# Performance work log

Hardware: AMD Instinct MI355X
Metric: run time of the kernel (lower is better)

## Reference

```python
import jax, jax.numpy as jnp
import numpy as np

N = 50000        # nodes
E = 800000       # edges (avg degree 16)
HID = 256        # hidden_size
HEADS = 8        # num_heads
HD = HID // HEADS  # head_dim = 32


def setup_inputs() -> dict:
    key = jax.random.key(0)
    ks = jax.random.split(key, 10)
    h = jax.random.normal(ks[0], (N, HID), dtype=jnp.float32)
    val = jax.random.uniform(ks[1], (E,), dtype=jnp.float32)
    Wq = jax.random.normal(ks[2], (HID, HID), dtype=jnp.float32) * 0.02
    Wk = jax.random.normal(ks[3], (HID, HID), dtype=jnp.float32) * 0.02
    Wv = jax.random.normal(ks[4], (HID, HID), dtype=jnp.float32) * 0.02
    bq = jnp.zeros((HID,), dtype=jnp.float32)
    bk = jnp.zeros((HID,), dtype=jnp.float32)
    bv = jnp.zeros((HID,), dtype=jnp.float32)
    # CSR rows expanded to per-edge row ids (sorted, like row_ptr expansion)
    edge_rows = jnp.sort(jax.random.randint(ks[5], (E,), 0, N, dtype=jnp.int32))
    col_ind = jax.random.randint(ks[6], (E,), 0, N, dtype=jnp.int32)
    return {"h": h, "val": val, "Wq": Wq, "bq": bq, "Wk": Wk, "bk": bk,
            "Wv": Wv, "bv": bv, "edge_rows": edge_rows, "col_ind": col_ind}


def reference(h, val, Wq, bq, Wk, bk, Wv, bv, edge_rows, col_ind):
    scaling = HD ** (-0.5)
    # projections; reshape splits hidden as (head_dim, heads) with heads fastest,
    # exactly as in the torch module: reshape(N, head_dim, num_heads)
    q = ((h @ Wq + bq).reshape(N, HD, HEADS)) * scaling
    k = (h @ Wk + bk).reshape(N, HD, HEADS)
    v = (h @ Wv + bv).reshape(N, HD, HEADS)

    # SDDMM restricted to edges: score[e, head] = <q[row_e], k[col_e]> * A.val[e]
    score = jnp.einsum('edh,edh->eh', q[edge_rows], k[col_ind]) * val[:, None]  # [E, HEADS]

    # per-destination-row softmax over incident edges (stable, segment ops)
    m = jax.ops.segment_max(score, edge_rows, num_segments=N)        # [N, HEADS]
    m = jnp.where(jnp.isfinite(m), m, jnp.zeros_like(m))             # empty rows
    e = jnp.exp(score - m[edge_rows])                                # [E, HEADS]
    denom = jax.ops.segment_sum(e, edge_rows, num_segments=N)        # [N, HEADS]
    attn = e / denom[edge_rows]

    # SpMM: out[i] = sum over edges (i, j) of attn * v[j]
    contrib = attn[:, None, :] * v[col_ind]                          # [E, HD, HEADS]
    out = jax.ops.segment_sum(contrib, edge_rows, num_segments=N)    # [N, HD, HEADS]
    return out.reshape(N, -1)                                        # [N, HID]
```

## Files before the change

### kernel.cpp

```cpp
#include <hip/hip_runtime.h>
#include <hip/hip_bf16.h>
#include <math.h>

static constexpr int kN   = 50000;
static constexpr int kE   = 800000;
static constexpr int kHID = 256;
static constexpr int kHD  = 32;

typedef short bf16x8 __attribute__((ext_vector_type(8)));
typedef float f32x4  __attribute__((ext_vector_type(4)));
typedef unsigned short us8 __attribute__((ext_vector_type(8)));

__device__ __forceinline__ float b2f(unsigned short u) {
  union { unsigned v; float f; } c; c.v = ((unsigned)u) << 16; return c.f;
}

__device__ __forceinline__ unsigned short f2bu(float f) {
  __hip_bfloat16 b = __float2bfloat16(f);
  union { __hip_bfloat16 b; unsigned short u; } c; c.b = b; return c.u;
}

__device__ __forceinline__ float quad_add_xor1(float s) {
  union { float f; int i; } a, b;
  a.f = s;
  b.i = __builtin_amdgcn_mov_dpp(a.i, 0xB1, 0xF, 0xF, true);
  return s + b.f;
}
__device__ __forceinline__ float quad_add_xor2(float s) {
  union { float f; int i; } a, b;
  a.f = s;
  b.i = __builtin_amdgcn_mov_dpp(a.i, 0x4E, 0xF, 0xF, true);
  return s + b.f;
}

__device__ __forceinline__ void load_lds16(const void* g, void* l) {
  __builtin_amdgcn_global_load_lds(
      (const __attribute__((address_space(1))) unsigned int*)(unsigned long long)(uintptr_t)g,
      (__attribute__((address_space(3))) unsigned int*)(unsigned int)(uintptr_t)l,
      16, 0, 0);
}

__global__ void split_h_kernel(const float* __restrict__ h,
                               __hip_bfloat16* __restrict__ Ah) {
  int idx = blockIdx.x * 256 + threadIdx.x;
  const f32x4* hp = (const f32x4*)(h + (size_t)idx * 8);
  f32x4 a = hp[0], b = hp[1];
  us8 o;
  o[0] = f2bu(a[0]); o[1] = f2bu(a[1]); o[2] = f2bu(a[2]); o[3] = f2bu(a[3]);
  o[4] = f2bu(b[0]); o[5] = f2bu(b[1]); o[6] = f2bu(b[2]); o[7] = f2bu(b[3]);
  *(us8*)(Ah + (size_t)idx * 8) = o;
}

__global__ void build_bt_kernel(const float* __restrict__ Wq, const float* __restrict__ bq,
                                const float* __restrict__ Wk, const float* __restrict__ bk,
                                const float* __restrict__ Wv, const float* __restrict__ bv,
                                __hip_bfloat16* __restrict__ Bt, float* __restrict__ biasP) {
  const int n  = blockIdx.x;
  const int kk = threadIdx.x;
  const int g  = n >> 8;
  const int cc = n & 255;
  const int c  = ((cc & 31) << 3) + (cc >> 5);
  const float scale = (g == 0) ? 0.17677669529663689f : 1.0f;
  const float* W = (g == 0) ? Wq : ((g == 1) ? Wk : Wv);
  Bt[n * 256 + kk] = __float2bfloat16(W[kk * 256 + c] * scale);
  if (kk == 0) {
    const float* b = (g == 0) ? bq : ((g == 1) ? bk : bv);
    biasP[n] = b[c] * scale;
  }
}

__global__ void build_row_ptr(const int* __restrict__ er, int* __restrict__ rp) {
  int i = blockIdx.x * blockDim.x + threadIdx.x;
  if (i > kN) return;
  int lo = 0, hi = kE;
  while (lo < hi) {
    int mid = (lo + hi) >> 1;
    if (er[mid] < i) lo = mid + 1; else hi = mid;
  }
  rp[i] = lo;
}

__global__ __launch_bounds__(256) void gemm_qkv_kernel(
    const __hip_bfloat16* __restrict__ Ah,
    const __hip_bfloat16* __restrict__ Bt, const float* __restrict__ biasP,
    __hip_bfloat16* __restrict__ qb, __hip_bfloat16* __restrict__ kvb) {
  __shared__ __align__(16) char smemRaw[34816];
  short* smemA = (short*)smemRaw;
  short* smemB = (short*)(smemRaw + 16384);
  short* smemC = (short*)smemRaw;

  const int L   = blockIdx.x;
  const int xcd = L & 7;
  const int t   = L >> 3;
  const int nt  = t % 6;
  const int mg  = t / 6;
  const int mt  = mg * 8 + xcd;
  if (mt >= 391) return;
  const int colBase = nt * 128;
  const int rowBase = mt * 128;

  const int tid  = threadIdx.x;
  const int wave = tid >> 6;
  const int lane = tid & 63;
  const int wm = wave & 1;
  const int wn = wave >> 1;

  f32x4 acc[4][4];
#pragma unroll
  for (int i = 0; i < 4; ++i)
#pragma unroll
    for (int j = 0; j < 4; ++j) acc[i][j] = f32x4{0.f, 0.f, 0.f, 0.f};

  for (int k0 = 0; k0 < 256; k0 += 64) {
    __syncthreads();
#pragma unroll
    for (int j = 0; j < 4; ++j) {
      int s = (wave * 4 + j) * 64 + lane;
      int r = s >> 3, cp = s & 7;
      int c = cp ^ (r & 7);
      int grow = rowBase + r;
      grow = grow < kN ? grow : kN - 1;
      const char* gp = (const char*)Ah + (size_t)grow * 512 + k0 * 2 + c * 16;
      load_lds16(gp, (char*)smemA + (wave * 4 + j) * 1024);
    }
#pragma unroll
    for (int j = 0; j < 4; ++j) {
      int s = (wave * 4 + j) * 64 + lane;
      int r = s >> 3, cp = s & 7;
      int c = cp ^ (r & 7);
      const char* gp = (const char*)Bt + (size_t)(colBase + r) * 512 + k0 * 2 + c * 16;
      load_lds16(gp, (char*)smemB + (wave * 4 + j) * 1024);
    }
    __syncthreads();

    const int rq = lane & 15, qd = lane >> 4;
#pragma unroll
    for (int ks = 0; ks < 2; ++ks) {
      bf16x8 af[4], bfr[4];
#pragma unroll
      for (int mi = 0; mi < 4; ++mi) {
        int r = wm * 64 + mi * 16 + rq;
        int c = (ks * 4 + qd) ^ (r & 7);
        af[mi] = *(const bf16x8*)&smemA[r * 64 + c * 8];
      }
#pragma unroll
      for (int nj = 0; nj < 4; ++nj) {
        int r = wn * 64 + nj * 16 + rq;
        int c = (ks * 4 + qd) ^ (r & 7);
        bfr[nj] = *(const bf16x8*)&smemB[r * 64 + c * 8];
      }
#pragma unroll
      for (int mi = 0; mi < 4; ++mi)
#pragma unroll
        for (int nj = 0; nj < 4; ++nj)
          acc[mi][nj] = __builtin_amdgcn_mfma_f32_16x16x32_bf16(
              af[mi], bfr[nj], acc[mi][nj], 0, 0, 0);
    }
  }

  __syncthreads();
#pragma unroll
  for (int nj = 0; nj < 4; ++nj) {
    const int cl = wn * 64 + nj * 16 + (lane & 15);
    const float bb = biasP[colBase + cl];
#pragma unroll
    for (int mi = 0; mi < 4; ++mi) {
      const int rl = wm * 64 + mi * 16 + (lane >> 4) * 4;
#pragma unroll
      for (int reg = 0; reg < 4; ++reg) {
        smemC[(rl + reg) * 136 + cl] = (short)f2bu(acc[mi][nj][reg] + bb);
      }
    }
  }
  __syncthreads();

  const int g = colBase >> 8;
#pragma unroll
  for (int it = 0; it < 8; ++it) {
    const int r   = it * 16 + (tid >> 4);
    const int c16 = tid & 15;
    const int row = rowBase + r;
    if (row < kN) {
      bf16x8 vls = *(const bf16x8*)&smemC[r * 136 + c16 * 8];
      const int cc = (colBase & 255) + c16 * 8;
      __hip_bfloat16* dst =
          (g == 0) ? (qb + (size_t)row * 256 + cc)
                   : (kvb + (size_t)row * 512 + (g == 2 ? 256 : 0) + cc);
      *(bf16x8*)dst = vls;
    }
  }
}

__global__ __launch_bounds__(256) void edge_attn_kernel(
    const __hip_bfloat16* __restrict__ qb, const __hip_bfloat16* __restrict__ kvb,
    const int* __restrict__ row_ptr, const int* __restrict__ col_ind,
    const float* __restrict__ val, float* __restrict__ out) {
  const int wave = threadIdx.x >> 6;
  const int lane = threadIdx.x & 63;
  const int half = lane >> 5;
  const int sl   = lane & 31;
  const int row = blockIdx.x * 4 + wave;
  if (row >= kN) return;

  const int e0 = row_ptr[row];
  const int e1 = row_ptr[row + 1];

  const us8 qu = *(const us8*)(qb + (size_t)row * 256 + sl * 8);
  float qf[8];
#pragma unroll
  for (int j = 0; j < 8; ++j) qf[j] = b2f(qu[j]) * 1.4426950408889634f;

  float denom = 0.f;
  float acc[8];
#pragma unroll
  for (int j = 0; j < 8; ++j) acc[j] = 0.f;

  if (e0 < e1) {
    const char* kvbL = (const char*)kvb + sl * 16;
    const int elast = e1 - 1;

    us8 kS[4], vS[4];
    float wS[4];
    int   colA[4], colB[4];
    float valA[4], valB[4];

    int c0[4]; float w0[4];
#pragma unroll
    for (int j = 0; j < 4; ++j) {
      const int ea = min(e0 + 2 * j + half, elast);
      c0[j] = col_ind[ea]; w0[j] = val[ea];
    }
#pragma unroll
    for (int j = 0; j < 4; ++j) {
      const int eb = min(e0 + 8 + 2 * j + half, elast);
      colA[j] = col_ind[eb]; valA[j] = val[eb];
    }
#pragma unroll
    for (int j = 0; j < 4; ++j) {
      const int ec = min(e0 + 16 + 2 * j + half, elast);
      colB[j] = col_ind[ec]; valB[j] = val[ec];
    }
#pragma unroll
    for (int j = 0; j < 4; ++j) {
      const size_t off = (size_t)c0[j] * 1024;
      kS[j] = *(const us8*)(kvbL + off);
      vS[j] = *(const us8*)(kvbL + off + 512);
      wS[j] = w0[j];
    }

#define ATTN_GROUP(EB, CB, VB)                                            \
    _Pragma("unroll")                                                     \
    for (int j = 0; j < 4; ++j) {                                         \
      const us8 kc = kS[j], vc = vS[j];                                   \
      const float wc = wS[j];                                             \
      {                                                                   \
        const size_t off = (size_t)CB[j] * 1024;                          \
        kS[j] = *(const us8*)(kvbL + off);                                \
        vS[j] = *(const us8*)(kvbL + off + 512);                          \
        wS[j] = VB[j];                                                    \
      }                                                                   \
      {                                                                   \
        const int en = min((EB) + 24 + 2 * j + half, elast);              \
        CB[j] = col_ind[en];                                              \
        VB[j] = val[en];                                                  \
      }                                                                   \
      float s = 0.f;                                                      \
      _Pragma("unroll")                                                   \
      for (int jj = 0; jj < 8; ++jj) s = fmaf(qf[jj], b2f(kc[jj]), s);    \
      s = quad_add_xor1(s);                                               \
      s = quad_add_xor2(s);                \
      s *= wc;                                                            \
      float p = exp2f(s);                                                 \
      p = (((EB) + 2 * j + half) < e1) ? p : 0.f;                         \
      denom += p;                                                         \
      _Pragma("unroll")                                                   \
      for (int jj = 0; jj < 8; ++jj) acc[jj] = fmaf(p, b2f(vc[jj]), acc[jj]); \
    }

    for (int e = e0; e < e1; e += 16) {
      ATTN_GROUP(e, colA, valA);
      ATTN_GROUP(e + 8, colB, valB);
    }
#undef ATTN_GROUP
  }

#pragma unroll
  for (int j = 0; j < 8; ++j) acc[j] += __shfl_xor(acc[j], 32);
  denom += __shfl_xor(denom, 32);

  const float inv = (denom > 0.f) ? (1.0f / denom) : 0.f;
  const int h = sl >> 2;
  const int dbase = (sl & 3) * 8 + half * 4;
  float* o = out + (size_t)row * 256 + h;
#pragma unroll
  for (int jj = 0; jj < 4; ++jj)
    o[(dbase + jj) * 8] = acc[half * 4 + jj] * inv;
}

extern "C" void kernel_launch(void* const* d_in, const int* in_sizes, int n_in,
                              void* d_out, int out_size, void* d_ws, size_t ws_size,
                              hipStream_t stream) {
  const float* h   = (const float*)d_in[0];
  const float* val = (const float*)d_in[1];
  const float* Wq  = (const float*)d_in[2];
  const float* bq  = (const float*)d_in[3];
  const float* Wk  = (const float*)d_in[4];
  const float* bk  = (const float*)d_in[5];
  const float* Wv  = (const float*)d_in[6];
  const float* bv  = (const float*)d_in[7];
  const int* edge_rows = (const int*)d_in[8];
  const int* col_ind   = (const int*)d_in[9];
  float* out = (float*)d_out;

  char* ws = (char*)d_ws;
  __hip_bfloat16* Ah  = (__hip_bfloat16*)ws;                 ws += (size_t)kN * 256 * 2;
  __hip_bfloat16* Bt  = (__hip_bfloat16*)ws;                 ws += (size_t)768 * 256 * 2;
  float*          biasP = (float*)ws;                        ws += 768 * 4;
  __hip_bfloat16* qb  = (__hip_bfloat16*)ws;                 ws += (size_t)kN * 256 * 2;
  __hip_bfloat16* kvb = (__hip_bfloat16*)ws;                 ws += (size_t)kN * 512 * 2;
  int* row_ptr = (int*)ws;

  split_h_kernel<<<kN / 8, 256, 0, stream>>>(h, Ah);
  build_bt_kernel<<<768, 256, 0, stream>>>(Wq, bq, Wk, bk, Wv, bv, Bt, biasP);
  build_row_ptr<<<(kN + 1 + 255) / 256, 256, 0, stream>>>(edge_rows, row_ptr);

  gemm_qkv_kernel<<<8 * 6 * 49, 256, 0, stream>>>(Ah, Bt, biasP, qb, kvb);

  edge_attn_kernel<<<(kN + 3) / 4, 256, 0, stream>>>(qb, kvb, row_ptr, col_ind,
                                                     val, out);
}
```

Before: 270.5 us.

## Make edge attention kernel persistent with cross-row software prefetch

The edge attention kernel becomes a grid-stride persistent kernel with 2048 blocks. Each wave walks several rows and prefetches the next row's row_ptr, q vector, first column indices and first K/V loads while the current row's softmax/SpMM runs. The aim is to hide gather latency at row boundaries and cut launch/tail cost, at the price of more registers and lower occupancy. Empty rows are handled with clamped indices and a zero denominator.

```diff
diff --git a/kernel.cpp b/kernel.cpp
--- a/kernel.cpp
+++ b/kernel.cpp
@@ -191,6 +191,9 @@
   }
 }
 
+static constexpr int kAttnBlocks = 2048;
+static constexpr int kAttnWaves  = kAttnBlocks * 4;
+
 __global__ __launch_bounds__(256) void edge_attn_kernel(
     const __hip_bfloat16* __restrict__ qb, const __hip_bfloat16* __restrict__ kvb,
     const int* __restrict__ row_ptr, const int* __restrict__ col_ind,
@@ -199,54 +202,67 @@
   const int lane = threadIdx.x & 63;
   const int half = lane >> 5;
   const int sl   = lane & 31;
-  const int row = blockIdx.x * 4 + wave;
-  if (row >= kN) return;
-
-  const int e0 = row_ptr[row];
-  const int e1 = row_ptr[row + 1];
-
-  const us8 qu = *(const us8*)(qb + (size_t)row * 256 + sl * 8);
-  float qf[8];
-#pragma unroll
-  for (int j = 0; j < 8; ++j) qf[j] = b2f(qu[j]) * 1.4426950408889634f;
-
-  float denom = 0.f;
-  float acc[8];
-#pragma unroll
-  for (int j = 0; j < 8; ++j) acc[j] = 0.f;
-
-  if (e0 < e1) {
-    const char* kvbL = (const char*)kvb + sl * 16;
-    const int elast = e1 - 1;
-
-    us8 kS[4], vS[4];
-    float wS[4];
-    int   colA[4], colB[4];
-    float valA[4], valB[4];
-
-    int c0[4]; float w0[4];
-#pragma unroll
-    for (int j = 0; j < 4; ++j) {
-      const int ea = min(e0 + 2 * j + half, elast);
-      c0[j] = col_ind[ea]; w0[j] = val[ea];
-    }
+  const char* kvbL = (const char*)kvb + sl * 16;
+
+  int r = blockIdx.x * 4 + wave;
+  if (r >= kN) return;
+
+  int eC0 = row_ptr[r], eC1 = row_ptr[r + 1];
+  int rn  = r + kAttnWaves;
+  int rnc = rn < kN ? rn : (kN - 1);
+  int eN0 = row_ptr[rnc], eN1 = row_ptr[rnc + 1];
+  us8 quC = *(const us8*)(qb + (size_t)r * 256 + sl * 8);
+
+  us8 kS[4], vS[4]; float wS[4];
+  {
+    const int elast = max(eC1 - 1, 0);
+#pragma unroll
+    for (int j = 0; j < 4; ++j) {
+      const int ea = min(eC0 + 2 * j + half, elast);
+      const int c = col_ind[ea];
+      wS[j] = val[ea];
+      const size_t off = (size_t)c * 1024;
+      kS[j] = *(const us8*)(kvbL + off);
+      vS[j] = *(const us8*)(kvbL + off + 512);
+    }
+  }
+
+  for (;;) {
+    const int e0 = eC0, e1 = eC1;
+    const int elast = max(e1 - 1, 0);
+
+    const int rnn  = r + 2 * kAttnWaves;
+    const int rnnc = rnn < kN ? rnn : (kN - 1);
+    const int eNN0 = row_ptr[rnnc], eNN1 = row_ptr[rnnc + 1];
+    const us8 quN  = *(const us8*)(qb + (size_t)rnc * 256 + sl * 8);
+    int c0N[4]; float w0N[4];
+    {
+      const int elN = max(eN1 - 1, 0);
+#pragma unroll
+      for (int j = 0; j < 4; ++j) {
+        const int en = min(eN0 + 2 * j + half, elN);
+        c0N[j] = col_ind[en];
+        w0N[j] = val[en];
+      }
+    }
+
+    int colA[4], colB[4]; float valA[4], valB[4];
 #pragma unroll
     for (int j = 0; j < 4; ++j) {
       const int eb = min(e0 + 8 + 2 * j + half, elast);
       colA[j] = col_ind[eb]; valA[j] = val[eb];
-    }
-#pragma unroll
-    for (int j = 0; j < 4; ++j) {
       const int ec = min(e0 + 16 + 2 * j + half, elast);
       colB[j] = col_ind[ec]; valB[j] = val[ec];
     }
-#pragma unroll
-    for (int j = 0; j < 4; ++j) {
-      const size_t off = (size_t)c0[j] * 1024;
-      kS[j] = *(const us8*)(kvbL + off);
-      vS[j] = *(const us8*)(kvbL + off + 512);
-      wS[j] = w0[j];
-    }
+
+    float qf[8];
+#pragma unroll
+    for (int j = 0; j < 8; ++j) qf[j] = b2f(quC[j]) * 1.4426950408889634f;
+
+    float denom = 0.f;
+    float acc[8];
+#pragma unroll
+    for (int j = 0; j < 8; ++j) acc[j] = 0.f;
 
 #define ATTN_GROUP(EB, CB, VB)                                            \
     _Pragma("unroll")                                                     \
@@ -282,19 +298,33 @@
       ATTN_GROUP(e + 8, colB, valB);
     }
 #undef ATTN_GROUP
-  }
-
-#pragma unroll
-  for (int j = 0; j < 8; ++j) acc[j] += __shfl_xor(acc[j], 32);
-  denom += __shfl_xor(denom, 32);
-
-  const float inv = (denom > 0.f) ? (1.0f / denom) : 0.f;
-  const int h = sl >> 2;
-  const int dbase = (sl & 3) * 8 + half * 4;
-  float* o = out + (size_t)row * 256 + h;
-#pragma unroll
-  for (int jj = 0; jj < 4; ++jj)
-    o[(dbase + jj) * 8] = acc[half * 4 + jj] * inv;
+
+#pragma unroll
+    for (int j = 0; j < 4; ++j) {
+      const size_t off = (size_t)c0N[j] * 1024;
+      kS[j] = *(const us8*)(kvbL + off);
+      vS[j] = *(const us8*)(kvbL + off + 512);
+      wS[j] = w0N[j];
+    }
+
+#pragma unroll
+    for (int j = 0; j < 8; ++j) acc[j] += __shfl_xor(acc[j], 32);
+    denom += __shfl_xor(denom, 32);
+    const float inv = (denom > 0.f) ? (1.0f / denom) : 0.f;
+    const int h = sl >> 2;
+    const int dbase = (sl & 3) * 8 + half * 4;
+    float* o = out + (size_t)r * 256 + h;
+#pragma unroll
+    for (int jj = 0; jj < 4; ++jj)
+      o[(dbase + jj) * 8] = acc[half * 4 + jj] * inv;
+
+    if (rn >= kN) break;
+    r   = rn;
+    eC0 = eN0; eC1 = eN1;
+    rn  = rnn; rnc = rnnc;
+    eN0 = eNN0; eN1 = eNN1;
+    quC = quN;
+  }
 }
 
 extern "C" void kernel_launch(void* const* d_in, const int* in_sizes, int n_in,
@@ -326,6 +356,6 @@
 
   gemm_qkv_kernel<<<8 * 6 * 49, 256, 0, stream>>>(Ah, Bt, biasP, qb, kvb);
 
-  edge_attn_kernel<<<(kN + 3) / 4, 256, 0, stream>>>(qb, kvb, row_ptr, col_ind,
-                                                     val, out);
-}
+  edge_attn_kernel<<<kAttnBlocks, 256, 0, stream>>>(qb, kvb, row_ptr, col_ind,
+                                                    val, out);
+}
```

Result: slower. 278.8 us (+3.1%).

## Interleave col/val into packed pairs, use packed-float math, shrink attention blocks

Applied to the files above, without the earlier changes.

Adds a prep kernel that interleaves col_ind and val into 8-byte pairs, so each edge's index and weight arrive in one load instead of two. The edge attention kernel now uses two-wide float vector operations for the dot product and accumulation, which the compiler may lower to packed FMA. It also runs 128-thread blocks with an occupancy hint. The cost is an extra pass over the edge arrays during prep, merged into the row_ptr kernel launch.

```diff
diff --git a/kernel.cpp b/kernel.cpp
--- a/kernel.cpp
+++ b/kernel.cpp
@@ -9,7 +9,11 @@
 
 typedef short bf16x8 __attribute__((ext_vector_type(8)));
 typedef float f32x4  __attribute__((ext_vector_type(4)));
+typedef float f32x2  __attribute__((ext_vector_type(2)));
 typedef unsigned short us8 __attribute__((ext_vector_type(8)));
+typedef unsigned int u32x4 __attribute__((ext_vector_type(4)));
+typedef int i32x2 __attribute__((ext_vector_type(2)));
+typedef int i32x4 __attribute__((ext_vector_type(4)));
 
 __device__ __forceinline__ float b2f(unsigned short u) {
   union { unsigned v; float f; } c; c.v = ((unsigned)u) << 16; return c.f;
@@ -18,6 +22,12 @@
 __device__ __forceinline__ unsigned short f2bu(float f) {
   __hip_bfloat16 b = __float2bfloat16(f);
   union { __hip_bfloat16 b; unsigned short u; } c; c.b = b; return c.u;
+}
+
+__device__ __forceinline__ f32x2 bf2up(unsigned u) {
+  union { unsigned v; float f; } lo, hi;
+  lo.v = u << 16; hi.v = u & 0xffff0000u;
+  return f32x2{lo.f, hi.f};
 }
 
 __device__ __forceinline__ float quad_add_xor1(float s) {
@@ -69,15 +79,30 @@
   }
 }
 
-__global__ void build_row_ptr(const int* __restrict__ er, int* __restrict__ rp) {
-  int i = blockIdx.x * blockDim.x + threadIdx.x;
-  if (i > kN) return;
-  int lo = 0, hi = kE;
-  while (lo < hi) {
-    int mid = (lo + hi) >> 1;
-    if (er[mid] < i) lo = mid + 1; else hi = mid;
-  }
-  rp[i] = lo;
+__global__ void prep_kernel(const int* __restrict__ er, int* __restrict__ rp,
+                            const int* __restrict__ ci, const float* __restrict__ vl,
+                            i32x2* __restrict__ cv) {
+  const int b = blockIdx.x;
+  if (b < 196) {
+    int i = b * 256 + threadIdx.x;
+    if (i > kN) return;
+    int lo = 0, hi = kE;
+    while (lo < hi) {
+      int mid = (lo + hi) >> 1;
+      if (er[mid] < i) lo = mid + 1; else hi = mid;
+    }
+    rp[i] = lo;
+  } else {
+    const int e4 = ((b - 196) * 256 + threadIdx.x) * 4;
+    if (e4 < kE) {
+      i32x4 c = *(const i32x4*)(ci + e4);
+      f32x4 w = *(const f32x4*)(vl + e4);
+      i32x4 o0 = {c[0], __float_as_int(w[0]), c[1], __float_as_int(w[1])};
+      i32x4 o1 = {c[2], __float_as_int(w[2]), c[3], __float_as_int(w[3])};
+      *(i32x4*)(cv + e4)     = o0;
+      *(i32x4*)(cv + e4 + 2) = o1;
+    }
+  }
 }
 
 __global__ __launch_bounds__(256) void gemm_qkv_kernel(
@@ -191,101 +216,110 @@
   }
 }
 
-__global__ __launch_bounds__(256) void edge_attn_kernel(
+__global__ __launch_bounds__(128, 7) void edge_attn_kernel(
     const __hip_bfloat16* __restrict__ qb, const __hip_bfloat16* __restrict__ kvb,
-    const int* __restrict__ row_ptr, const int* __restrict__ col_ind,
-    const float* __restrict__ val, float* __restrict__ out) {
+    const int* __restrict__ row_ptr, const i32x2* __restrict__ cvp,
+    float* __restrict__ out) {
   const int wave = threadIdx.x >> 6;
   const int lane = threadIdx.x & 63;
   const int half = lane >> 5;
   const int sl   = lane & 31;
-  const int row = blockIdx.x * 4 + wave;
+  const int row = blockIdx.x * 2 + wave;
   if (row >= kN) return;
 
   const int e0 = row_ptr[row];
   const int e1 = row_ptr[row + 1];
 
   const us8 qu = *(const us8*)(qb + (size_t)row * 256 + sl * 8);
-  float qf[8];
-#pragma unroll
-  for (int j = 0; j < 8; ++j) qf[j] = b2f(qu[j]) * 1.4426950408889634f;
+  f32x2 qf2[4];
+#pragma unroll
+  for (int j = 0; j < 4; ++j)
+    qf2[j] = f32x2{b2f(qu[2 * j]) * 1.4426950408889634f,
+                   b2f(qu[2 * j + 1]) * 1.4426950408889634f};
 
   float denom = 0.f;
-  float acc[8];
-#pragma unroll
-  for (int j = 0; j < 8; ++j) acc[j] = 0.f;
+  f32x2 acc2[4];
+#pragma unroll
+  for (int j = 0; j < 4; ++j) acc2[j] = f32x2{0.f, 0.f};
 
   if (e0 < e1) {
     const char* kvbL = (const char*)kvb + sl * 16;
     const int elast = e1 - 1;
 
-    us8 kS[4], vS[4];
+    u32x4 kS[4], vS[4];
     float wS[4];
-    int   colA[4], colB[4];
-    float valA[4], valB[4];
-
-    int c0[4]; float w0[4];
+    i32x2 cvA[4], cvB[4];
+
+    i32x2 c0[4];
 #pragma unroll
     for (int j = 0; j < 4; ++j) {
       const int ea = min(e0 + 2 * j + half, elast);
-      c0[j] = col_ind[ea]; w0[j] = val[ea];
+      c0[j] = cvp[ea];
     }
 #pragma unroll
     for (int j = 0; j < 4; ++j) {
       const int eb = min(e0 + 8 + 2 * j + half, elast);
-      colA[j] = col_ind[eb]; valA[j] = val[eb];
+      cvA[j] = cvp[eb];
     }
 #pragma unroll
     for (int j = 0; j < 4; ++j) {
       const int ec = min(e0 + 16 + 2 * j + half, elast);
-      colB[j] = col_ind[ec]; valB[j] = val[ec];
-    }
-#pragma unroll
-    for (int j = 0; j < 4; ++j) {
-      const size_t off = (size_t)c0[j] * 1024;
-      kS[j] = *(const us8*)(kvbL + off);
-      vS[j] = *(const us8*)(kvbL + off + 512);
-      wS[j] = w0[j];
-    }
-
-#define ATTN_GROUP(EB, CB, VB)                                            \
+      cvB[j] = cvp[ec];
+    }
+#pragma unroll
+    for (int j = 0; j < 4; ++j) {
+      const size_t off = (size_t)c0[j][0] * 1024;
+      kS[j] = *(const u32x4*)(kvbL + off);
+      vS[j] = *(const u32x4*)(kvbL + off + 512);
+      wS[j] = __int_as_float(c0[j][1]);
+    }
+
+#define ATTN_GROUP(EB, CB)                                                \
     _Pragma("unroll")                                                     \
     for (int j = 0; j < 4; ++j) {                                         \
-      const us8 kc = kS[j], vc = vS[j];                                   \
+      const u32x4 kc = kS[j], vc = vS[j];                                 \
       const float wc = wS[j];                                             \
       {                                                                   \
-        const size_t off = (size_t)CB[j] * 1024;                          \
-        kS[j] = *(const us8*)(kvbL + off);                                \
-        vS[j] = *(const us8*)(kvbL + off + 512);                          \
-        wS[j] = VB[j];                                                    \
+        const size_t off = (size_t)CB[j][0] * 1024;                       \
+        kS[j] = *(const u32x4*)(kvbL + off);                              \
+        vS[j] = *(const u32x4*)(kvbL + off + 512);                        \
+        wS[j] = __int_as_float(CB[j][1]);                                 \
       }                                                                   \
       {                                                                   \
         const int en = min((EB) + 24 + 2 * j + half, elast);              \
-        CB[j] = col_ind[en];                                              \
-        VB[j] = val[en];                                                  \
+        CB[j] = cvp[en];                                                  \
       }                                                                   \
-      float s = 0.f;                                                      \
-      _Pragma("unroll")                                                   \
-      for (int jj = 0; jj < 8; ++jj) s = fmaf(qf[jj], b2f(kc[jj]), s);    \
+      f32x2 s2 = qf2[0] * bf2up(kc[0]);                                   \
+      s2 += qf2[1] * bf2up(kc[1]);                                        \
+      s2 += qf2[2] * bf2up(kc[2]);                                        \
+      s2 += qf2[3] * bf2up(kc[3]);                                        \
+      float s = s2[0] + s2[1];                                            \
       s = quad_add_xor1(s);                                               \
       s = quad_add_xor2(s);                \
       s *= wc;                                                            \
       float p = exp2f(s);                                                 \
       p = (((EB) + 2 * j + half) < e1) ? p : 0.f;                         \
       denom += p;                                                         \
-      _Pragma("unroll")                                                   \
-      for (int jj = 0; jj < 8; ++jj) acc[jj] = fmaf(p, b2f(vc[jj]), acc[jj]); \
+      const f32x2 p2 = {p, p};                                            \
+      acc2[0] += p2 * bf2up(vc[0]);                                       \
+      acc2[1] += p2 * bf2up(vc[1]);                                       \
+      acc2[2] += p2 * bf2up(vc[2]);                                       \
+      acc2[3] += p2 * bf2up(vc[3]);                                       \
     }
 
     for (int e = e0; e < e1; e += 16) {
-      ATTN_GROUP(e, colA, valA);
-      ATTN_GROUP(e + 8, colB, valB);
+      ATTN_GROUP(e, cvA);
+      ATTN_GROUP(e + 8, cvB);
     }
 #undef ATTN_GROUP
   }
 
-#pragma unroll
-  for (int j = 0; j < 8; ++j) acc[j] += __shfl_xor(acc[j], 32);
+  float accs[8];
+#pragma unroll
+  for (int j = 0; j < 8; ++j) {
+    float a = (j & 1) ? acc2[j >> 1][1] : acc2[j >> 1][0];
+    accs[j] = a + __shfl_xor(a, 32);
+  }
   denom += __shfl_xor(denom, 32);
 
   const float inv = (denom > 0.f) ? (1.0f / denom) : 0.f;
@@ -294,7 +328,7 @@
   float* o = out + (size_t)row * 256 + h;
 #pragma unroll
   for (int jj = 0; jj < 4; ++jj)
-    o[(dbase + jj) * 8] = acc[half * 4 + jj] * inv;
+    o[(dbase + jj) * 8] = accs[half * 4 + jj] * inv;
 }
 
 extern "C" void kernel_launch(void* const* d_in, const int* in_sizes, int n_in,
@@ -318,14 +352,14 @@
   float*          biasP = (float*)ws;                        ws += 768 * 4;
   __hip_bfloat16* qb  = (__hip_bfloat16*)ws;                 ws += (size_t)kN * 256 * 2;
   __hip_bfloat16* kvb = (__hip_bfloat16*)ws;                 ws += (size_t)kN * 512 * 2;
-  int* row_ptr = (int*)ws;
+  int* row_ptr = (int*)ws;                                   ws += ((size_t)(kN + 1) * 4 + 127) & ~127ull;
+  i32x2* cv = (i32x2*)ws;
 
   split_h_kernel<<<kN / 8, 256, 0, stream>>>(h, Ah);
   build_bt_kernel<<<768, 256, 0, stream>>>(Wq, bq, Wk, bk, Wv, bv, Bt, biasP);
-  build_row_ptr<<<(kN + 1 + 255) / 256, 256, 0, stream>>>(edge_rows, row_ptr);
+  prep_kernel<<<196 + 782, 256, 0, stream>>>(edge_rows, row_ptr, col_ind, val, cv);
 
   gemm_qkv_kernel<<<8 * 6 * 49, 256, 0, stream>>>(Ah, Bt, biasP, qb, kvb);
 
-  edge_attn_kernel<<<(kN + 3) / 4, 256, 0, stream>>>(qb, kvb, row_ptr, col_ind,
-                                                     val, out);
-}
+  edge_attn_kernel<<<(kN + 1) / 2, 128, 0, stream>>>(qb, kvb, row_ptr, cv, out);
+}
```

Result: slower. 452.5 us (+67.3%).
